# Kernel optimization log

Hardware: AMD Instinct MI355X
Metric: run time of the kernel (lower is better)

Reference implementation:

```python
import jax, jax.numpy as jnp
import numpy as np

NUM_GAUSSIANS = 20
NUM_LETTERS = 80
HIDDEN_SIZE = 400
ATTENTION_SCALE = 0.05
B, U = 1024, 1024


def setup_inputs() -> dict:
    key = jax.random.key(0)
    k1, k2, k3, k4, k5 = jax.random.split(key, 5)
    text_inputs = jax.random.randint(k1, (B, U), 0, NUM_LETTERS)          # [B, U] int
    text_lengths = jax.random.randint(k2, (B,), 0, U)                     # [B] int
    y_0 = jax.random.normal(k3, (B, HIDDEN_SIZE), dtype=jnp.float32)      # [B, H]
    prev_k = jax.random.uniform(k4, (B, NUM_GAUSSIANS), dtype=jnp.float32)  # [B, N]
    # window_layer params: Linear(H, 3N)
    kw, kb = jax.random.split(k5)
    lim = 1.0 / np.sqrt(HIDDEN_SIZE)
    W = jax.random.uniform(kw, (3 * NUM_GAUSSIANS, HIDDEN_SIZE), minval=-lim, maxval=lim, dtype=jnp.float32)
    bias = jax.random.uniform(kb, (3 * NUM_GAUSSIANS,), minval=-lim, maxval=lim, dtype=jnp.float32)
    return {"text_inputs": text_inputs, "text_lengths": text_lengths,
            "y_0": y_0, "prev_k": prev_k, "W": W, "bias": bias}


def reference(text_inputs, text_lengths, y_0, prev_k, W, bias):
    N = prev_k.shape[1]
    batch, maxlen = text_inputs.shape
    out = y_0 @ W.T + bias                                   # [B, 3N]
    a = jnp.exp(out[:, :N])[..., None]                       # [B, N, 1]
    b = jnp.exp(out[:, N:2 * N])[..., None]                  # [B, N, 1]
    k = (jnp.exp(out[:, 2 * N:]) * ATTENTION_SCALE + prev_k)[..., None]  # [B, N, 1]
    u = jnp.arange(maxlen, dtype=out.dtype)[None, None, :]   # [1, 1, U]
    text_mask = (jnp.arange(maxlen)[None, :] < text_lengths[:, None]).astype(out.dtype)  # [B, U]
    phi_t_u = jnp.sum(a * jnp.exp(-b * (k - u) ** 2), axis=1) * text_mask  # [B, U]
    # w_t = sum_u one_hot(text)[b,u,:] * phi[b,u]  ==  scatter-add over letter dim
    rows = jnp.arange(batch)[:, None]                        # [B, 1]
    w_t = jnp.zeros((batch, NUM_LETTERS), dtype=out.dtype).at[rows, text_inputs].add(phi_t_u)  # [B, L]
    return (w_t, k[..., 0], phi_t_u)
```

## Files before the change

kernel.cpp:

```cpp
#include <hip/hip_runtime.h>

#define NG 20
#define NL 80
#define HS 400
#define ASCALE 0.05f
#define BB 1024
#define UU 1024
#define LOG2E 1.4426950408889634f

__global__ __launch_bounds__(256, 4) void window_fused_kernel(
    const int*   __restrict__ text,
    const int*   __restrict__ tlen,
    const float* __restrict__ y0,
    const float* __restrict__ prevk,
    const float* __restrict__ W,
    const float* __restrict__ bias,
    float* __restrict__ w_t,
    float* __restrict__ k_out,
    float* __restrict__ phi_out)
{
    const int b   = blockIdx.x;
    const int tid = threadIdx.x;

    const int4 letters = reinterpret_cast<const int4*>(text + b * UU)[tid];
    const int  len     = tlen[b];

    __shared__ float yrow[HS];
    __shared__ float LAs[NG], B2s[NG], Ks[NG];
    __shared__ float wloc[NL];

    if (tid < HS / 4) {
        reinterpret_cast<float4*>(yrow)[tid] =
            reinterpret_cast<const float4*>(y0 + b * HS)[tid];
    }
    if (tid < NL) wloc[tid] = 0.f;
    __syncthreads();

    if (tid < 3 * NG * 4) {
        const int j = tid >> 2;
        const int p = tid & 3;
        const float4* wr = reinterpret_cast<const float4*>(W + j * HS + p * 100);
        const float4* yr = reinterpret_cast<const float4*>(yrow + p * 100);
        float s = 0.f;
        #pragma unroll 5
        for (int i = 0; i < 25; ++i) {
            const float4 w4 = wr[i];
            const float4 y4 = yr[i];
            s += w4.x * y4.x + w4.y * y4.y + w4.z * y4.z + w4.w * y4.w;
        }
        s += __shfl_down(s, 1, 4);
        s += __shfl_down(s, 2, 4);
        if (p == 0) {
            const float val = s + bias[j];
            if (j < NG) {
                LAs[j] = val * LOG2E;
            } else if (j < 2 * NG) {
                B2s[j - NG] = __expf(val) * LOG2E;
            } else {
                const int g = j - 2 * NG;
                const float kk = __expf(val) * ASCALE + prevk[b * NG + g];
                Ks[g] = kk;
                k_out[b * NG + g] = kk;
            }
        }
    }
    __syncthreads();

    float la[NG], b2[NG], kg[NG];
    #pragma unroll
    for (int n = 0; n < NG; ++n) { la[n] = LAs[n]; b2[n] = B2s[n]; kg[n] = Ks[n]; }

    const int u0 = tid * 4;
    float s0 = 0.f, s1 = 0.f, s2 = 0.f, s3 = 0.f;
    if (u0 < len) {
        const float uf = (float)u0;
        #pragma unroll
        for (int n = 0; n < NG; ++n) {
            const float d0 = kg[n] - uf;
            const float d1 = d0 - 1.f;
            const float d2 = d0 - 2.f;
            const float d3 = d0 - 3.f;
            s0 += __builtin_amdgcn_exp2f(__builtin_fmaf(-b2[n] * d0, d0, la[n]));
            s1 += __builtin_amdgcn_exp2f(__builtin_fmaf(-b2[n] * d1, d1, la[n]));
            s2 += __builtin_amdgcn_exp2f(__builtin_fmaf(-b2[n] * d2, d2, la[n]));
            s3 += __builtin_amdgcn_exp2f(__builtin_fmaf(-b2[n] * d3, d3, la[n]));
        }
        if (u0 + 1 >= len) s1 = 0.f;
        if (u0 + 2 >= len) s2 = 0.f;
        if (u0 + 3 >= len) s3 = 0.f;
    }
    float4 phi4; phi4.x = s0; phi4.y = s1; phi4.z = s2; phi4.w = s3;
    reinterpret_cast<float4*>(phi_out + b * UU)[tid] = phi4;

    if (s0 != 0.f) atomicAdd(&wloc[letters.x], s0);
    if (s1 != 0.f) atomicAdd(&wloc[letters.y], s1);
    if (s2 != 0.f) atomicAdd(&wloc[letters.z], s2);
    if (s3 != 0.f) atomicAdd(&wloc[letters.w], s3);
    __syncthreads();

    if (tid < NL) w_t[b * NL + tid] = wloc[tid];
}

extern "C" void kernel_launch(void* const* d_in, const int* in_sizes, int n_in,
                              void* d_out, int out_size, void* d_ws, size_t ws_size,
                              hipStream_t stream) {
    const int*   text  = (const int*)  d_in[0];
    const int*   tlen  = (const int*)  d_in[1];
    const float* y0    = (const float*)d_in[2];
    const float* prevk = (const float*)d_in[3];
    const float* W     = (const float*)d_in[4];
    const float* bias  = (const float*)d_in[5];

    float* out   = (float*)d_out;
    float* w_t   = out;
    float* k_out = out + BB * NL;
    float* phi   = out + BB * NL + BB * NG;

    hipLaunchKernelGGL(window_fused_kernel, dim3(BB), dim3(256), 0, stream,
                       text, tlen, y0, prevk, W, bias, w_t, k_out, phi);
}
```

Baseline: 75.69 us.

## Split parameter GEMV into separate kernel reusing W across four batch rows

Moves the linear-layer projection out of the fused window kernel into its own kernel. There each block keeps its slice of W in registers and applies it to four y rows, so W is reread from memory a quarter as often. The window kernel now reads the precomputed per-row parameters from a workspace buffer. This adds a second kernel launch and a round trip through global memory, and the register-held W may lower occupancy of the parameter kernel.

```diff
diff --git a/kernel.cpp b/kernel.cpp
--- a/kernel.cpp
+++ b/kernel.cpp
@@ -8,15 +8,70 @@
 #define UU 1024
 #define LOG2E 1.4426950408889634f
 
-__global__ __launch_bounds__(256, 4) void window_fused_kernel(
-    const int*   __restrict__ text,
-    const int*   __restrict__ tlen,
+__global__ __launch_bounds__(256, 2) void param_kernel(
     const float* __restrict__ y0,
     const float* __restrict__ prevk,
     const float* __restrict__ W,
     const float* __restrict__ bias,
+    float* __restrict__ params,
+    float* __restrict__ k_out)
+{
+    const int rb  = blockIdx.x * 4;
+    const int tid = threadIdx.x;
+
+    __shared__ float yrow[4][HS];
+
+    for (int i = tid; i < 4 * HS / 4; i += 256) {
+        reinterpret_cast<float4*>(&yrow[0][0])[i] =
+            reinterpret_cast<const float4*>(y0 + rb * HS)[i];
+    }
+    __syncthreads();
+
+    if (tid < 3 * NG * 4) {
+        const int j = tid >> 2;
+        const int p = tid & 3;
+        float4 wreg[25];
+        const float4* wr = reinterpret_cast<const float4*>(W + j * HS + p * 100);
+        #pragma unroll
+        for (int i = 0; i < 25; ++i) wreg[i] = wr[i];
+        const float bj = bias[j];
+
+        #pragma unroll
+        for (int r = 0; r < 4; ++r) {
+            const float4* yr = reinterpret_cast<const float4*>(&yrow[r][p * 100]);
+            float s = 0.f;
+            #pragma unroll
+            for (int i = 0; i < 25; ++i) {
+                const float4 w4 = wreg[i];
+                const float4 y4 = yr[i];
+                s += w4.x * y4.x + w4.y * y4.y + w4.z * y4.z + w4.w * y4.w;
+            }
+            s += __shfl_down(s, 1, 4);
+            s += __shfl_down(s, 2, 4);
+            if (p == 0) {
+                const int row = rb + r;
+                const float val = s + bj;
+                float outv;
+                if (j < NG) {
+                    outv = val * LOG2E;
+                } else if (j < 2 * NG) {
+                    outv = __expf(val) * LOG2E;
+                } else {
+                    const int g = j - 2 * NG;
+                    outv = __expf(val) * ASCALE + prevk[row * NG + g];
+                    k_out[row * NG + g] = outv;
+                }
+                params[row * 60 + j] = outv;
+            }
+        }
+    }
+}
+
+__global__ __launch_bounds__(256, 4) void window_kernel(
+    const int*   __restrict__ text,
+    const int*   __restrict__ tlen,
+    const float* __restrict__ params,
     float* __restrict__ w_t,
-    float* __restrict__ k_out,
     float* __restrict__ phi_out)
 {
     const int b   = blockIdx.x;
@@ -25,50 +80,18 @@
     const int4 letters = reinterpret_cast<const int4*>(text + b * UU)[tid];
     const int  len     = tlen[b];
 
-    __shared__ float yrow[HS];
-    __shared__ float LAs[NG], B2s[NG], Ks[NG];
     __shared__ float wloc[NL];
+    if (tid < NL) wloc[tid] = 0.f;
 
-    if (tid < HS / 4) {
-        reinterpret_cast<float4*>(yrow)[tid] =
-            reinterpret_cast<const float4*>(y0 + b * HS)[tid];
-    }
-    if (tid < NL) wloc[tid] = 0.f;
-    __syncthreads();
-
-    if (tid < 3 * NG * 4) {
-        const int j = tid >> 2;
-        const int p = tid & 3;
-        const float4* wr = reinterpret_cast<const float4*>(W + j * HS + p * 100);
-        const float4* yr = reinterpret_cast<const float4*>(yrow + p * 100);
-        float s = 0.f;
-        #pragma unroll 5
-        for (int i = 0; i < 25; ++i) {
-            const float4 w4 = wr[i];
-            const float4 y4 = yr[i];
-            s += w4.x * y4.x + w4.y * y4.y + w4.z * y4.z + w4.w * y4.w;
-        }
-        s += __shfl_down(s, 1, 4);
-        s += __shfl_down(s, 2, 4);
-        if (p == 0) {
-            const float val = s + bias[j];
-            if (j < NG) {
-                LAs[j] = val * LOG2E;
-            } else if (j < 2 * NG) {
-                B2s[j - NG] = __expf(val) * LOG2E;
-            } else {
-                const int g = j - 2 * NG;
-                const float kk = __expf(val) * ASCALE + prevk[b * NG + g];
-                Ks[g] = kk;
-                k_out[b * NG + g] = kk;
-            }
-        }
+    const float* pp = params + b * 60;
+    float la[NG], b2[NG], kg[NG];
+    #pragma unroll
+    for (int n = 0; n < NG; ++n) {
+        la[n] = pp[n];
+        b2[n] = pp[NG + n];
+        kg[n] = pp[2 * NG + n];
     }
     __syncthreads();
-
-    float la[NG], b2[NG], kg[NG];
-    #pragma unroll
-    for (int n = 0; n < NG; ++n) { la[n] = LAs[n]; b2[n] = B2s[n]; kg[n] = Ks[n]; }
 
     const int u0 = tid * 4;
     float s0 = 0.f, s1 = 0.f, s2 = 0.f, s3 = 0.f;
@@ -111,11 +134,14 @@
     const float* W     = (const float*)d_in[4];
     const float* bias  = (const float*)d_in[5];
 
-    float* out   = (float*)d_out;
-    float* w_t   = out;
-    float* k_out = out + BB * NL;
-    float* phi   = out + BB * NL + BB * NG;
+    float* out    = (float*)d_out;
+    float* w_t    = out;
+    float* k_out  = out + BB * NL;
+    float* phi    = out + BB * NL + BB * NG;
+    float* params = (float*)d_ws;
 
-    hipLaunchKernelGGL(window_fused_kernel, dim3(BB), dim3(256), 0, stream,
-                       text, tlen, y0, prevk, W, bias, w_t, k_out, phi);
+    hipLaunchKernelGGL(param_kernel, dim3(BB / 4), dim3(256), 0, stream,
+                       y0, prevk, W, bias, params, k_out);
+    hipLaunchKernelGGL(window_kernel, dim3(BB), dim3(256), 0, stream,
+                       text, tlen, params, w_t, phi);
 }
```

After: 76.90 us. About the same (+1.6%).

## Use 512-thread blocks with 2 outputs per thread and 8-way GEMV split

Applied to the files above, without the earlier changes.

Doubles the block size to 512 threads so each thread computes two phi positions instead of four. The 60x400 window GEMV is split eight ways per output instead of four, using two accumulators and a three-step shuffle reduction. The Gaussian parameters are packed as float4 in shared memory and read during the loop instead of being held in registers. This aims to cut the serial GEMV prologue and per-thread work and to raise occupancy, at the cost of more threads per block and narrower memory accesses.

```diff
diff --git a/kernel.cpp b/kernel.cpp
--- a/kernel.cpp
+++ b/kernel.cpp
@@ -8,7 +8,7 @@
 #define UU 1024
 #define LOG2E 1.4426950408889634f
 
-__global__ __launch_bounds__(256, 4) void window_fused_kernel(
+__global__ __launch_bounds__(512, 8) void window_fused512(
     const int*   __restrict__ text,
     const int*   __restrict__ tlen,
     const float* __restrict__ y0,
@@ -22,11 +22,11 @@
     const int b   = blockIdx.x;
     const int tid = threadIdx.x;
 
-    const int4 letters = reinterpret_cast<const int4*>(text + b * UU)[tid];
+    const int2 letters = reinterpret_cast<const int2*>(text + b * UU)[tid];
     const int  len     = tlen[b];
 
-    __shared__ float yrow[HS];
-    __shared__ float LAs[NG], B2s[NG], Ks[NG];
+    __shared__ __align__(16) float yrow[HS];
+    __shared__ __align__(16) float p4s[NG * 4];
     __shared__ float wloc[NL];
 
     if (tid < HS / 4) {
@@ -36,66 +36,62 @@
     if (tid < NL) wloc[tid] = 0.f;
     __syncthreads();
 
-    if (tid < 3 * NG * 4) {
-        const int j = tid >> 2;
-        const int p = tid & 3;
-        const float4* wr = reinterpret_cast<const float4*>(W + j * HS + p * 100);
-        const float4* yr = reinterpret_cast<const float4*>(yrow + p * 100);
-        float s = 0.f;
-        #pragma unroll 5
-        for (int i = 0; i < 25; ++i) {
-            const float4 w4 = wr[i];
-            const float4 y4 = yr[i];
-            s += w4.x * y4.x + w4.y * y4.y + w4.z * y4.z + w4.w * y4.w;
+    if (tid < 3 * NG * 8) {
+        const int j = tid >> 3;
+        const int p = tid & 7;
+        const float2* wr = reinterpret_cast<const float2*>(W + j * HS + p * 50);
+        const float2* yr = reinterpret_cast<const float2*>(yrow + p * 50);
+        float sa = 0.f, sb = 0.f;
+        #pragma unroll
+        for (int i = 0; i < 24; i += 2) {
+            const float2 w0 = wr[i],     yv0 = yr[i];
+            const float2 w1 = wr[i + 1], yv1 = yr[i + 1];
+            sa += w0.x * yv0.x + w0.y * yv0.y;
+            sb += w1.x * yv1.x + w1.y * yv1.y;
         }
-        s += __shfl_down(s, 1, 4);
-        s += __shfl_down(s, 2, 4);
+        {
+            const float2 w0 = wr[24], yv0 = yr[24];
+            sa += w0.x * yv0.x + w0.y * yv0.y;
+        }
+        float s = sa + sb;
+        s += __shfl_down(s, 1, 8);
+        s += __shfl_down(s, 2, 8);
+        s += __shfl_down(s, 4, 8);
         if (p == 0) {
             const float val = s + bias[j];
             if (j < NG) {
-                LAs[j] = val * LOG2E;
+                p4s[j * 4 + 0] = val * LOG2E;
             } else if (j < 2 * NG) {
-                B2s[j - NG] = __expf(val) * LOG2E;
+                p4s[(j - NG) * 4 + 1] = __expf(val) * LOG2E;
             } else {
                 const int g = j - 2 * NG;
                 const float kk = __expf(val) * ASCALE + prevk[b * NG + g];
-                Ks[g] = kk;
+                p4s[g * 4 + 2] = kk;
                 k_out[b * NG + g] = kk;
             }
         }
     }
     __syncthreads();
 
-    float la[NG], b2[NG], kg[NG];
-    #pragma unroll
-    for (int n = 0; n < NG; ++n) { la[n] = LAs[n]; b2[n] = B2s[n]; kg[n] = Ks[n]; }
-
-    const int u0 = tid * 4;
-    float s0 = 0.f, s1 = 0.f, s2 = 0.f, s3 = 0.f;
+    const int u0 = tid * 2;
+    float s0 = 0.f, s1 = 0.f;
     if (u0 < len) {
         const float uf = (float)u0;
         #pragma unroll
         for (int n = 0; n < NG; ++n) {
-            const float d0 = kg[n] - uf;
+            const float4 g = reinterpret_cast<const float4*>(p4s)[n];
+            const float d0 = g.z - uf;
             const float d1 = d0 - 1.f;
-            const float d2 = d0 - 2.f;
-            const float d3 = d0 - 3.f;
-            s0 += __builtin_amdgcn_exp2f(__builtin_fmaf(-b2[n] * d0, d0, la[n]));
-            s1 += __builtin_amdgcn_exp2f(__builtin_fmaf(-b2[n] * d1, d1, la[n]));
-            s2 += __builtin_amdgcn_exp2f(__builtin_fmaf(-b2[n] * d2, d2, la[n]));
-            s3 += __builtin_amdgcn_exp2f(__builtin_fmaf(-b2[n] * d3, d3, la[n]));
+            s0 += __builtin_amdgcn_exp2f(__builtin_fmaf(-g.y * d0, d0, g.x));
+            s1 += __builtin_amdgcn_exp2f(__builtin_fmaf(-g.y * d1, d1, g.x));
         }
         if (u0 + 1 >= len) s1 = 0.f;
-        if (u0 + 2 >= len) s2 = 0.f;
-        if (u0 + 3 >= len) s3 = 0.f;
     }
-    float4 phi4; phi4.x = s0; phi4.y = s1; phi4.z = s2; phi4.w = s3;
-    reinterpret_cast<float4*>(phi_out + b * UU)[tid] = phi4;
+    float2 phi2; phi2.x = s0; phi2.y = s1;
+    reinterpret_cast<float2*>(phi_out + b * UU)[tid] = phi2;
 
     if (s0 != 0.f) atomicAdd(&wloc[letters.x], s0);
     if (s1 != 0.f) atomicAdd(&wloc[letters.y], s1);
-    if (s2 != 0.f) atomicAdd(&wloc[letters.z], s2);
-    if (s3 != 0.f) atomicAdd(&wloc[letters.w], s3);
     __syncthreads();
 
     if (tid < NL) w_t[b * NL + tid] = wloc[tid];
@@ -116,6 +112,6 @@
     float* k_out = out + BB * NL;
     float* phi   = out + BB * NL + BB * NG;
 
-    hipLaunchKernelGGL(window_fused_kernel, dim3(BB), dim3(256), 0, stream,
+    hipLaunchKernelGGL(window_fused512, dim3(BB), dim3(512), 0, stream,
                        text, tlen, y0, prevk, W, bias, w_t, k_out, phi);
 }
```

Measured after the change: 76.58 us. Within noise of the previous version (+1.2%).
